# Performance work log

Hardware: AMD Instinct MI355X
Metric: run time of the kernel (lower is better)

## Reference

```python
import math
import jax, jax.numpy as jnp
import numpy as np

B, T, D = 2, 2048, 1024
NH = 16
HD = D // NH


def setup_inputs() -> dict:
    key = jax.random.key(0)
    k1, k2, k3 = jax.random.split(key, 3)
    s = 0.02
    return {
        "x": jax.random.normal(k1, (B, T, D), dtype=jnp.float32),
        "w_qkv": jax.random.normal(k2, (D, 3 * D), dtype=jnp.float32) * s,
        "w_proj": jax.random.normal(k3, (D, D), dtype=jnp.float32) * s,
    }


def reference(x, w_qkv, w_proj):
    b, t, c = x.shape
    qkv = x @ w_qkv  # [B,T,3D]
    q, k, v = jnp.split(qkv, 3, axis=-1)
    # [B,NH,T,HD]
    q = q.reshape(b, t, NH, HD).transpose(0, 2, 1, 3)
    k = k.reshape(b, t, NH, HD).transpose(0, 2, 1, 3)
    v = v.reshape(b, t, NH, HD).transpose(0, 2, 1, 3)
    scores = jnp.einsum("bhqd,bhkd->bhqk", q, k) / math.sqrt(HD)
    mask = jnp.tril(jnp.ones((t, t), dtype=x.dtype))  # [T,T]
    # faithful to source: scaled scores are multiplied by the mask, then -1e9 added where masked
    masked = scores * mask + (1.0 - mask) * (-1e9)
    a = jax.nn.softmax(masked, axis=-1)
    out = jnp.einsum("bhqk,bhkd->bhqd", a, v)  # [B,NH,T,HD]
    out = out.transpose(0, 2, 1, 3).reshape(b, t, c)
    return out @ w_proj
```

## Files before the change

kernel.cpp:

```cpp
#include <hip/hip_runtime.h>
#include <stdint.h>

#define B_SZ 2
#define T_SEQ 2048
#define D_MODEL 1024
#define NHEADS 16
#define HDIM 64
#define QKV_P (3 * D_MODEL)

typedef unsigned short u16;
typedef uint32_t u32;
typedef __attribute__((ext_vector_type(4))) float f32x4;
typedef __attribute__((ext_vector_type(8))) short s16x8;
typedef __attribute__((ext_vector_type(4))) short s16x4;

__device__ __forceinline__ u16 f2bf(float f) {
  union { float f; uint32_t u; } v; v.f = f;
  uint32_t r = v.u + 0x7fffu + ((v.u >> 16) & 1u);
  return (u16)(r >> 16);
}

__device__ __forceinline__ float fastexp2(float x) {
  float r;
  asm volatile("v_exp_f32 %0, %1" : "=v"(r) : "v"(x));
  return r;
}

__device__ __forceinline__ u32 cvtpk(float lo, float hi) {
  u32 r;
  asm volatile("v_cvt_pk_bf16_f32 %0, %1, %2" : "=v"(r) : "v"(lo), "v"(hi));
  return r;
}

__device__ __forceinline__ void async16(const void* g, void* l) {
  __builtin_amdgcn_global_load_lds((const __attribute__((address_space(1))) void*)g,
                                   (__attribute__((address_space(3))) void*)l,
                                   16, 0, 0);
}

__global__ __launch_bounds__(256) void prep(const float* __restrict__ x,
                                            const float* __restrict__ wq,
                                            const float* __restrict__ wp,
                                            u16* __restrict__ xb,
                                            u16* __restrict__ wqkvT,
                                            u16* __restrict__ wprojT) {
  const int bid = blockIdx.x, tid = threadIdx.x;
  if (bid < 4096) {
    int i = bid * 256 + tid;
    float4 v = ((const float4*)x)[i];
    ushort4 o;
    o.x = f2bf(v.x); o.y = f2bf(v.y); o.z = f2bf(v.z); o.w = f2bf(v.w);
    ((ushort4*)xb)[i] = o;
    return;
  }
  __shared__ float tile[32][33];
  const float* in; u16* outp; int C, bx, by;
  if (bid < 4096 + 3072) {
    int bb = bid - 4096; in = wq; outp = wqkvT; C = 3072; bx = bb % 96; by = bb / 96;
  } else {
    int bb = bid - 7168; in = wp; outp = wprojT; C = 1024; bx = bb % 32; by = bb / 32;
  }
  const int tx = tid & 31, ty = tid >> 5;
  const int c0 = bx * 32, r0 = by * 32;
#pragma unroll
  for (int i = 0; i < 4; i++)
    tile[ty + i * 8][tx] = in[(size_t)(r0 + ty + i * 8) * C + c0 + tx];
  __syncthreads();
#pragma unroll
  for (int i = 0; i < 4; i++)
    outp[(size_t)(c0 + ty + i * 8) * D_MODEL + r0 + tx] = f2bf(tile[tx][ty + i * 8]);
}

template <int F32OUT, int VFUSE>
__global__ __launch_bounds__(256) void gemm_bt(const u16* __restrict__ A,
                                               const u16* __restrict__ BT,
                                               void* __restrict__ Cout,
                                               u16* __restrict__ vTout,
                                               int M, int N, int K) {
  __shared__ u16 As[2][128 * 32];
  __shared__ u16 Bs[2][128 * 32];
  const int tid = threadIdx.x;
  const int lane = tid & 63, w = tid >> 6;
  const int l15 = lane & 15, g = lane >> 4;
  const int wr = w >> 1, wc = w & 1;
  const int bn = blockIdx.x, bm = blockIdx.y;
  const u16* Ab = A + (size_t)bm * 128 * K;
  const u16* Bb = BT + (size_t)bn * 128 * K;
  f32x4 acc[4][4];
#pragma unroll
  for (int i = 0; i < 4; i++)
#pragma unroll
    for (int j = 0; j < 4; j++) acc[i][j] = (f32x4){0.f, 0.f, 0.f, 0.f};
  const int c0 = tid, c1 = tid + 256;

#define GSTAGE(buf, kt_)                                                          \
  do {                                                                            \
    async16(Ab + (size_t)(c0 >> 2) * K + (kt_) + (c0 & 3) * 8, (char*)As[buf] + c0 * 16); \
    async16(Ab + (size_t)(c1 >> 2) * K + (kt_) + (c1 & 3) * 8, (char*)As[buf] + c1 * 16); \
    async16(Bb + (size_t)(c0 >> 2) * K + (kt_) + (c0 & 3) * 8, (char*)Bs[buf] + c0 * 16); \
    async16(Bb + (size_t)(c1 >> 2) * K + (kt_) + (c1 & 3) * 8, (char*)Bs[buf] + c1 * 16); \
  } while (0)

  GSTAGE(0, 0);
  int cur = 0;
  for (int kt = 0; kt < K; kt += 32) {
    if (kt + 32 < K) {
      GSTAGE(cur ^ 1, kt + 32);
      asm volatile("s_waitcnt vmcnt(4)" ::: "memory");
    } else {
      asm volatile("s_waitcnt vmcnt(0)" ::: "memory");
    }
    __syncthreads();
    s16x8 af[4], bfr[4];
#pragma unroll
    for (int i = 0; i < 4; i++)
      af[i] = *(const s16x8*)(As[cur] + (wr * 64 + i * 16 + l15) * 32 + g * 8);
#pragma unroll
    for (int j = 0; j < 4; j++)
      bfr[j] = *(const s16x8*)(Bs[cur] + (wc * 64 + j * 16 + l15) * 32 + g * 8);
#pragma unroll
    for (int i = 0; i < 4; i++)
#pragma unroll
      for (int j = 0; j < 4; j++)
        acc[i][j] = __builtin_amdgcn_mfma_f32_16x16x32_bf16(af[i], bfr[j], acc[i][j], 0, 0, 0);
    __syncthreads();
    cur ^= 1;
  }

  if (VFUSE && bn >= 16) {
    const int bloc = bm >> 4;
    const int tb = bm * 128 + wr * 64 - bloc * T_SEQ;
#pragma unroll
    for (int i = 0; i < 4; i++) {
      const int tl = tb + i * 16 + g * 4;
#pragma unroll
      for (int j = 0; j < 4; j++) {
        const int hh = bn * 128 + wc * 64 + j * 16 + l15 - 2048;
        uint2 pk;
        pk.x = cvtpk(acc[i][j][0], acc[i][j][1]);
        pk.y = cvtpk(acc[i][j][2], acc[i][j][3]);
        *(uint2*)&vTout[(size_t)(bloc * 1024 + hh) * T_SEQ + tl] = pk;
      }
    }
    return;
  }
#pragma unroll
  for (int i = 0; i < 4; i++) {
    const int row0 = bm * 128 + wr * 64 + i * 16 + g * 4;
#pragma unroll
    for (int j = 0; j < 4; j++) {
      const int col = bn * 128 + wc * 64 + j * 16 + l15;
#pragma unroll
      for (int r = 0; r < 4; r++) {
        if (F32OUT)
          ((float*)Cout)[(size_t)(row0 + r) * N + col] = acc[i][j][r];
        else
          ((u16*)Cout)[(size_t)(row0 + r) * N + col] = f2bf(acc[i][j][r]);
      }
    }
  }
}

__global__ __launch_bounds__(256, 4) void flash_attn(const u16* __restrict__ qkv,
                                                     const u16* __restrict__ vT,
                                                     u16* __restrict__ attn) {
  __shared__ u16 Ks[2][64 * 64];
  __shared__ u16 Vs[2][64 * 64];
  const int tid = threadIdx.x;
  const int lane = tid & 63, w = tid >> 6;
  const int l15 = lane & 15, g = lane >> 4;
  const int id = blockIdx.x;
  const int bh = ((id & 7) << 2) | ((id >> 3) & 3);
  const int j = (id >> 5) & 7, k4 = (id >> 8) & 3;
  const int qs = (k4 == 0) ? (31 - j) : (k4 == 1) ? (16 + j) : (k4 == 2) ? (15 - j) : j;
  const int b = bh >> 4, h = bh & 15;

  const size_t qrow = (size_t)(b * T_SEQ + qs * 64 + w * 16 + l15);
  s16x8 qf[2];
  qf[0] = *(const s16x8*)(qkv + qrow * QKV_P + h * HDIM + 0 * 32 + g * 8);
  qf[1] = *(const s16x8*)(qkv + qrow * QKV_P + h * HDIM + 1 * 32 + g * 8);

  f32x4 O[4];
#pragma unroll
  for (int t = 0; t < 4; t++) O[t] = (f32x4){0.f, 0.f, 0.f, 0.f};
  float m_s = -1e30f, l_s = 0.f;
  const int qrl = w * 16 + l15;
  const float sc = 0.18033688011112042f;

#define STAGE(buf, kvt_)                                                                     \
  do {                                                                                       \
    _Pragma("unroll") for (int i_ = 0; i_ < 2; i_++) {                                       \
      int o_ = (tid + i_ * 256) * 16;                                                        \
      int lo_ = o_ ^ (((o_ >> 7) & 7) << 4);                                                 \
      int row_ = lo_ >> 7;                                                                   \
      int byt_ = lo_ & 127;                                                                  \
      async16(qkv + (size_t)(b * T_SEQ + (kvt_) * 64 + row_) * QKV_P + D_MODEL + h * HDIM +  \
                  (byt_ >> 1),                                                               \
              (char*)Ks[buf] + o_);                                                          \
      async16(vT + (size_t)(bh * HDIM + row_) * T_SEQ + (kvt_) * 64 + (byt_ >> 1),           \
              (char*)Vs[buf] + o_);                                                          \
    }                                                                                        \
  } while (0)

  STAGE(0, 0);
  int cur = 0;
  const int nt = qs + 1;
  for (int kvt = 0; kvt < nt; ++kvt) {
    if (kvt < qs) {
      STAGE(cur ^ 1, kvt + 1);
      asm volatile("s_waitcnt vmcnt(4)" ::: "memory");
    } else {
      asm volatile("s_waitcnt vmcnt(0)" ::: "memory");
    }
    __syncthreads();

    f32x4 S[4];
#pragma unroll
    for (int t16 = 0; t16 < 4; t16++) S[t16] = (f32x4){0.f, 0.f, 0.f, 0.f};
#pragma unroll
    for (int t16 = 0; t16 < 4; t16++)
#pragma unroll
      for (int kk = 0; kk < 2; kk++) {
        int key = t16 * 16 + l15;
        int bp = (key * 128 + kk * 64 + g * 16) ^ ((key & 7) << 4);
        s16x8 kf = *(const s16x8*)((const char*)Ks[cur] + bp);
        S[t16] = __builtin_amdgcn_mfma_f32_16x16x32_bf16(kf, qf[kk], S[t16], 0, 0, 0);
      }

    if (kvt == qs) {
#pragma unroll
      for (int t16 = 0; t16 < 4; t16++)
#pragma unroll
        for (int r = 0; r < 4; r++)
          if (t16 * 16 + g * 4 + r > qrl) S[t16][r] = -3e38f;
    }
    float mx = fmaxf(fmaxf(fmaxf(S[0][0], S[0][1]), fmaxf(S[0][2], S[0][3])),
                     fmaxf(fmaxf(S[1][0], S[1][1]), fmaxf(S[1][2], S[1][3])));
    mx = fmaxf(mx, fmaxf(fmaxf(fmaxf(S[2][0], S[2][1]), fmaxf(S[2][2], S[2][3])),
                         fmaxf(fmaxf(S[3][0], S[3][1]), fmaxf(S[3][2], S[3][3]))));
    mx = fmaxf(mx, __shfl_xor(mx, 16));
    mx = fmaxf(mx, __shfl_xor(mx, 32));
    if (!__all(mx - m_s <= 40.f)) {
      const float mnew = fmaxf(m_s, mx);
      const float alpha = fastexp2((m_s - mnew) * sc);
      m_s = mnew;
      l_s *= alpha;
#pragma unroll
      for (int t = 0; t < 4; t++)
#pragma unroll
        for (int r = 0; r < 4; r++) O[t][r] *= alpha;
    }
    const float msc = m_s * sc;
    float p[16];
#pragma unroll
    for (int t16 = 0; t16 < 4; t16++)
#pragma unroll
      for (int r = 0; r < 4; r++) p[t16 * 4 + r] = fastexp2(fmaf(S[t16][r], sc, -msc));
    float ps = 0.f;
#pragma unroll
    for (int i = 0; i < 16; i++) ps += p[i];
    ps += __shfl_xor(ps, 16);
    ps += __shfl_xor(ps, 32);
    l_s += ps;

#pragma unroll
    for (int t16 = 0; t16 < 4; t16++) {
      union { u32 u[2]; s16x4 v; } pbv;
      pbv.u[0] = cvtpk(p[t16 * 4 + 0], p[t16 * 4 + 1]);
      pbv.u[1] = cvtpk(p[t16 * 4 + 2], p[t16 * 4 + 3]);
#pragma unroll
      for (int t = 0; t < 4; t++) {
        int hd = t * 16 + l15;
        int bp = (hd * 128 + t16 * 32 + g * 8) ^ ((hd & 7) << 4);
        s16x4 vf = *(const s16x4*)((const char*)Vs[cur] + bp);
        O[t] = __builtin_amdgcn_mfma_f32_16x16x16bf16_1k(vf, pbv.v, O[t], 0, 0, 0);
      }
    }
    __syncthreads();
    cur ^= 1;
  }

  const float inv = 1.0f / l_s;
  const size_t row = (size_t)(b * T_SEQ + qs * 64 + w * 16 + l15);
#pragma unroll
  for (int t = 0; t < 4; t++)
#pragma unroll
    for (int pr = 0; pr < 2; pr++) {
      u32 pk = cvtpk(O[t][pr * 2 + 0] * inv, O[t][pr * 2 + 1] * inv);
      *(u32*)&attn[row * D_MODEL + h * HDIM + t * 16 + g * 4 + pr * 2] = pk;
    }
}

extern "C" void kernel_launch(void* const* d_in, const int* in_sizes, int n_in,
                              void* d_out, int out_size, void* d_ws, size_t ws_size,
                              hipStream_t stream) {
  const float* x = (const float*)d_in[0];
  const float* w_qkv = (const float*)d_in[1];
  const float* w_proj = (const float*)d_in[2];
  float* out = (float*)d_out;
  char* ws = (char*)d_ws;
  const size_t MB = (size_t)1 << 20;
  if (ws_size < 56 * MB) return;
  u16* xb = (u16*)(ws + 0);
  u16* wqkvT = (u16*)(ws + 8 * MB);
  u16* wprojT = (u16*)(ws + 14 * MB);
  u16* qkv = (u16*)(ws + 16 * MB);
  u16* vT = (u16*)(ws + 40 * MB);
  u16* attn = (u16*)(ws + 48 * MB);

  prep<<<8192, 256, 0, stream>>>(x, w_qkv, w_proj, xb, wqkvT, wprojT);
  gemm_bt<0, 1><<<dim3(QKV_P / 128, (B_SZ * T_SEQ) / 128), 256, 0, stream>>>(
      xb, wqkvT, qkv, vT, B_SZ * T_SEQ, QKV_P, D_MODEL);
  flash_attn<<<1024, 256, 0, stream>>>(qkv, vT, attn);
  gemm_bt<1, 0><<<dim3(D_MODEL / 128, (B_SZ * T_SEQ) / 128), 256, 0, stream>>>(
      attn, wprojT, out, nullptr, B_SZ * T_SEQ, D_MODEL, D_MODEL);
}
```

Baseline: 114.2 us.

## Replace QKV GEMM with 256x256-tile, 512-thread kernel using swizzled LDS

New measurement: 134.4 us. +17.7%, slower.

```diff
diff --git a/kernel.cpp b/kernel.cpp
--- a/kernel.cpp
+++ b/kernel.cpp
@@ -71,12 +71,149 @@
     outp[(size_t)(c0 + ty + i * 8) * D_MODEL + r0 + tx] = f2bf(tile[tx][ty + i * 8]);
 }
 
-template <int F32OUT, int VFUSE>
-__global__ __launch_bounds__(256) void gemm_bt(const u16* __restrict__ A,
-                                               const u16* __restrict__ BT,
-                                               void* __restrict__ Cout,
-                                               u16* __restrict__ vTout,
-                                               int M, int N, int K) {
+__global__ __launch_bounds__(512, 1) void gemm_qkv(const u16* __restrict__ A,
+                                                   const u16* __restrict__ BT,
+                                                   u16* __restrict__ qkv,
+                                                   u16* __restrict__ vTout) {
+  __shared__ u16 As[2][256 * 64];
+  __shared__ u16 Bs[2][256 * 64];
+  const int tid = threadIdx.x;
+  const int lane = tid & 63, w = tid >> 6;
+  const int l15 = lane & 15, g = lane >> 4;
+  const int wr = w >> 2, wc = w & 3;
+  const int id = blockIdx.x;
+  const int swz = (id & 7) * 24 + (id >> 3);
+  const int bm = swz / 12, bn = swz % 12;
+  const int K = 1024;
+  const u16* Ab = A + (size_t)bm * 256 * K;
+  const u16* Bb = BT + (size_t)bn * 256 * K;
+
+  f32x4 acc[8][4];
+#pragma unroll
+  for (int i = 0; i < 8; i++)
+#pragma unroll
+    for (int j = 0; j < 4; j++) acc[i][j] = (f32x4){0.f, 0.f, 0.f, 0.f};
+
+#define HT2(dst, srcb, i0, kt_)                                                       \
+  do {                                                                                \
+    _Pragma("unroll") for (int i_ = (i0); i_ < (i0) + 2; i_++) {                      \
+      int c_ = tid + i_ * 512;                                                        \
+      int o_ = c_ * 16;                                                               \
+      int lo_ = o_ ^ (((o_ >> 7) & 7) << 4);                                          \
+      async16((srcb) + (size_t)(lo_ >> 7) * K + (kt_) + ((lo_ & 127) >> 1),           \
+              (char*)(dst) + o_);                                                     \
+    }                                                                                 \
+  } while (0)
+
+#define AFR(dstf, i_, kk_)                                                            \
+  {                                                                                   \
+    int r_ = wr * 128 + (i_)*16 + l15;                                                \
+    int bp_ = (r_ * 128 + (kk_)*64 + g * 16) ^ ((r_ & 7) << 4);                       \
+    dstf = *(const s16x8*)((const char*)As[cur] + bp_);                               \
+  }
+#define BFR(dstf, j_, kk_)                                                            \
+  {                                                                                   \
+    int n_ = wc * 64 + (j_)*16 + l15;                                                 \
+    int bp_ = (n_ * 128 + (kk_)*64 + g * 16) ^ ((n_ & 7) << 4);                       \
+    dstf = *(const s16x8*)((const char*)Bs[cur] + bp_);                               \
+  }
+
+  HT2(As[0], Ab, 0, 0);
+  HT2(As[0], Ab, 2, 0);
+  HT2(Bs[0], Bb, 0, 0);
+  HT2(Bs[0], Bb, 2, 0);
+  int cur = 0;
+
+  for (int t = 0; t < 16; t++) {
+    const int ktn = (t + 1) * 64;
+    const bool pf = (t < 15);
+    s16x8 bf[4][2], af[2][2];
+
+    if (pf) {
+      HT2(As[cur ^ 1], Ab, 0, ktn);
+      asm volatile("s_waitcnt vmcnt(2)" ::: "memory");
+    } else {
+      asm volatile("s_waitcnt vmcnt(0)" ::: "memory");
+    }
+    __syncthreads();
+#pragma unroll
+    for (int j = 0; j < 4; j++) {
+      BFR(bf[j][0], j, 0);
+      BFR(bf[j][1], j, 1);
+    }
+    AFR(af[0][0], 0, 0); AFR(af[0][1], 0, 1);
+    AFR(af[1][0], 1, 0); AFR(af[1][1], 1, 1);
+    __builtin_amdgcn_s_setprio(1);
+#pragma unroll
+    for (int i = 0; i < 2; i++)
+#pragma unroll
+      for (int j = 0; j < 4; j++) {
+        acc[i][j] = __builtin_amdgcn_mfma_f32_16x16x32_bf16(af[i][0], bf[j][0], acc[i][j], 0, 0, 0);
+        acc[i][j] = __builtin_amdgcn_mfma_f32_16x16x32_bf16(af[i][1], bf[j][1], acc[i][j], 0, 0, 0);
+      }
+    __builtin_amdgcn_s_setprio(0);
+    __syncthreads();
+
+#pragma unroll
+    for (int p = 1; p < 4; p++) {
+      if (pf) {
+        if (p == 1) HT2(As[cur ^ 1], Ab, 2, ktn);
+        if (p == 2) HT2(Bs[cur ^ 1], Bb, 0, ktn);
+        if (p == 3) HT2(Bs[cur ^ 1], Bb, 2, ktn);
+      }
+      AFR(af[0][0], 2 * p, 0); AFR(af[0][1], 2 * p, 1);
+      AFR(af[1][0], 2 * p + 1, 0); AFR(af[1][1], 2 * p + 1, 1);
+      __syncthreads();
+      __builtin_amdgcn_s_setprio(1);
+#pragma unroll
+      for (int i = 0; i < 2; i++)
+#pragma unroll
+        for (int j = 0; j < 4; j++) {
+          acc[2 * p + i][j] =
+              __builtin_amdgcn_mfma_f32_16x16x32_bf16(af[i][0], bf[j][0], acc[2 * p + i][j], 0, 0, 0);
+          acc[2 * p + i][j] =
+              __builtin_amdgcn_mfma_f32_16x16x32_bf16(af[i][1], bf[j][1], acc[2 * p + i][j], 0, 0, 0);
+        }
+      __builtin_amdgcn_s_setprio(0);
+      __syncthreads();
+    }
+    cur ^= 1;
+  }
+
+  if (bn >= 8) {
+#pragma unroll
+    for (int i = 0; i < 8; i++) {
+      const int m = bm * 256 + wr * 128 + i * 16 + g * 4;
+      const int bloc = m >> 11;
+      const int tl = m & 2047;
+#pragma unroll
+      for (int j = 0; j < 4; j++) {
+        const int hh = bn * 256 + wc * 64 + j * 16 + l15 - 2048;
+        uint2 pk;
+        pk.x = cvtpk(acc[i][j][0], acc[i][j][1]);
+        pk.y = cvtpk(acc[i][j][2], acc[i][j][3]);
+        *(uint2*)&vTout[(size_t)(bloc * 1024 + hh) * T_SEQ + tl] = pk;
+      }
+    }
+    return;
+  }
+#pragma unroll
+  for (int i = 0; i < 8; i++) {
+    const int row0 = bm * 256 + wr * 128 + i * 16 + g * 4;
+#pragma unroll
+    for (int j = 0; j < 4; j++) {
+      const int col = bn * 256 + wc * 64 + j * 16 + l15;
+#pragma unroll
+      for (int r = 0; r < 4; r++)
+        qkv[(size_t)(row0 + r) * QKV_P + col] = f2bf(acc[i][j][r]);
+    }
+  }
+}
+
+__global__ __launch_bounds__(256) void gemm_proj(const u16* __restrict__ A,
+                                                 const u16* __restrict__ BT,
+                                                 float* __restrict__ Cout,
+                                                 int M, int N, int K) {
   __shared__ u16 As[2][128 * 32];
   __shared__ u16 Bs[2][128 * 32];
   const int tid = threadIdx.x;
@@ -93,8 +230,8 @@
     for (int j = 0; j < 4; j++) acc[i][j] = (f32x4){0.f, 0.f, 0.f, 0.f};
   const int c0 = tid, c1 = tid + 256;
 
-#define GSTAGE(buf, kt_)                                                          \
-  do {                                                                            \
+#define GSTAGE(buf, kt_)                                                                  \
+  do {                                                                                    \
     async16(Ab + (size_t)(c0 >> 2) * K + (kt_) + (c0 & 3) * 8, (char*)As[buf] + c0 * 16); \
     async16(Ab + (size_t)(c1 >> 2) * K + (kt_) + (c1 & 3) * 8, (char*)As[buf] + c1 * 16); \
     async16(Bb + (size_t)(c0 >> 2) * K + (kt_) + (c0 & 3) * 8, (char*)Bs[buf] + c0 * 16); \
@@ -126,24 +263,6 @@
     __syncthreads();
     cur ^= 1;
   }
-
-  if (VFUSE && bn >= 16) {
-    const int bloc = bm >> 4;
-    const int tb = bm * 128 + wr * 64 - bloc * T_SEQ;
-#pragma unroll
-    for (int i = 0; i < 4; i++) {
-      const int tl = tb + i * 16 + g * 4;
-#pragma unroll
-      for (int j = 0; j < 4; j++) {
-        const int hh = bn * 128 + wc * 64 + j * 16 + l15 - 2048;
-        uint2 pk;
-        pk.x = cvtpk(acc[i][j][0], acc[i][j][1]);
-        pk.y = cvtpk(acc[i][j][2], acc[i][j][3]);
-        *(uint2*)&vTout[(size_t)(bloc * 1024 + hh) * T_SEQ + tl] = pk;
-      }
-    }
-    return;
-  }
 #pragma unroll
   for (int i = 0; i < 4; i++) {
     const int row0 = bm * 128 + wr * 64 + i * 16 + g * 4;
@@ -151,12 +270,8 @@
     for (int j = 0; j < 4; j++) {
       const int col = bn * 128 + wc * 64 + j * 16 + l15;
 #pragma unroll
-      for (int r = 0; r < 4; r++) {
-        if (F32OUT)
-          ((float*)Cout)[(size_t)(row0 + r) * N + col] = acc[i][j][r];
-        else
-          ((u16*)Cout)[(size_t)(row0 + r) * N + col] = f2bf(acc[i][j][r]);
-      }
+      for (int r = 0; r < 4; r++)
+        Cout[(size_t)(row0 + r) * N + col] = acc[i][j][r];
     }
   }
 }
@@ -309,9 +424,8 @@
   u16* attn = (u16*)(ws + 48 * MB);
 
   prep<<<8192, 256, 0, stream>>>(x, w_qkv, w_proj, xb, wqkvT, wprojT);
-  gemm_bt<0, 1><<<dim3(QKV_P / 128, (B_SZ * T_SEQ) / 128), 256, 0, stream>>>(
-      xb, wqkvT, qkv, vT, B_SZ * T_SEQ, QKV_P, D_MODEL);
+  gemm_qkv<<<192, 512, 0, stream>>>(xb, wqkvT, qkv, vT);
   flash_attn<<<1024, 256, 0, stream>>>(qkv, vT, attn);
-  gemm_bt<1, 0><<<dim3(D_MODEL / 128, (B_SZ * T_SEQ) / 128), 256, 0, stream>>>(
-      attn, wprojT, out, nullptr, B_SZ * T_SEQ, D_MODEL, D_MODEL);
-}
+  gemm_proj<<<dim3(D_MODEL / 128, (B_SZ * T_SEQ) / 128), 256, 0, stream>>>(
+      attn, wprojT, out, B_SZ * T_SEQ, D_MODEL, D_MODEL);
+}
```
